# Optimization experiments

Measured on AMD Instinct MI355X. Metric: run time of the kernel, lower is better.

Reference implementation:

```python
import jax, jax.numpy as jnp
import numpy as np
from jax import lax

B, NS, SL, NF = 1024, 9, 36, 7
H, DM, DH, FFN = 2, 128, 64, 2048
EPS = 1e-5


def setup_inputs():
    ks = jax.random.split(jax.random.key(0), 12)
    r = lambda i, shape, s=0.05: jax.random.normal(ks[i], shape, dtype=jnp.float32) * s
    return {
        "x": jax.random.normal(ks[0], (B, NS, SL, NF), dtype=jnp.float32),
        "W_g1": r(1, (NS, 64)), "b_g1": jnp.zeros((64,), jnp.float32),
        "W_g2": r(2, (64, DM)), "b_g2": jnp.zeros((DM,), jnp.float32),
        "conv1_w": r(3, (64, NF, 5)), "conv1_b": jnp.zeros((64,), jnp.float32),
        "conv2_w": r(4, (DM, 64, 3)), "conv2_b": jnp.zeros((DM,), jnp.float32),
        "bn_g": jnp.ones((DM,), jnp.float32), "bn_b": jnp.zeros((DM,), jnp.float32),
        "bn_m": jnp.zeros((DM,), jnp.float32), "bn_v": jnp.ones((DM,), jnp.float32),
        "in_proj_w": r(5, (2, 3 * DM, DM)), "in_proj_b": jnp.zeros((2, 3 * DM), jnp.float32),
        "out_proj_w": r(6, (2, DM, DM)), "out_proj_b": jnp.zeros((2, DM), jnp.float32),
        "ln1_g": jnp.ones((2, DM), jnp.float32), "ln1_b": jnp.zeros((2, DM), jnp.float32),
        "ln2_g": jnp.ones((2, DM), jnp.float32), "ln2_b": jnp.zeros((2, DM), jnp.float32),
        "ffn_w1": r(7, (2, FFN, DM)), "ffn_b1": jnp.zeros((2, FFN), jnp.float32),
        "ffn_w2": r(8, (2, DM, FFN)), "ffn_b2": jnp.zeros((2, DM), jnp.float32),
        "attn_w": r(9, (DM, 1)), "attn_b": jnp.zeros((1,), jnp.float32),
        "fc_w": r(10, (DM, 1)), "fc_b": jnp.zeros((1,), jnp.float32),
    }


def _ln(z, g, b):
    m = jnp.mean(z, -1, keepdims=True)
    v = jnp.mean(jnp.square(z - m), -1, keepdims=True)
    return (z - m) * lax.rsqrt(v + EPS) * g + b


def _gcn_agg(h):
    # Fully-connected 9-node graph (softmax(adj) > 0 everywhere, incl. self loops):
    # GCN norm deg=9 -> rows 0..8 become the mean of rows 0..8.
    # Remaining rows only receive the add_remaining_self_loops self loop (deg=1) -> identity.
    return h.at[:NS].set(jnp.mean(h[:NS], axis=0, keepdims=True))


def _forward(x, W_g1, b_g1, W_g2, b_g2, conv1_w, conv1_b, conv2_w, conv2_b,
             bn_g, bn_b, bn_m, bn_v, in_proj_w, in_proj_b, out_proj_w, out_proj_b,
             ln1_g, ln1_b, ln2_g, ln2_b, ffn_w1, ffn_b1, ffn_w2, ffn_b2,
             attn_w, attn_b, fc_w, fc_b):
    Bx = x.shape[0]
    # ---- GCN branch (edge weights from softmax(adj) are never used by GCNConv) ----
    xg = jnp.mean(x, axis=-1).reshape(Bx * SL, NS)                 # (B*36, 9)
    h = jax.nn.relu(_gcn_agg(xg @ W_g1) + b_g1)                    # (B*36, 64)
    h = jax.nn.relu(_gcn_agg(h @ W_g2) + b_g2)                     # (B*36, 128)
    x_gcn = h.reshape(Bx, SL, DM)
    # ---- conv branch ----
    xc = x.reshape(Bx * NS, NF, SL)
    dn = ("NCH", "OIH", "NCH")
    c = lax.conv_general_dilated(xc, conv1_w, (1,), [(2, 2)], dimension_numbers=dn) + conv1_b[:, None]
    c = lax.conv_general_dilated(c, conv2_w, (1,), [(1, 1)], dimension_numbers=dn) + conv2_b[:, None]
    c = (c - bn_m[:, None]) * lax.rsqrt(bn_v[:, None] + EPS) * bn_g[:, None] + bn_b[:, None]
    # AdaptiveAvgPool1d(36) on length-36 input is identity; eval-mode dropout is identity.
    s = c.reshape(Bx, NS, DM, SL).mean(axis=1).transpose(0, 2, 1)  # (B, 36, 128) batch-first
    # ---- post-LN transformer encoder (torch defaults, eval mode) ----
    scale = 1.0 / np.sqrt(DH).astype(np.float32)
    for i in range(2):
        qkv = s @ in_proj_w[i].T + in_proj_b[i]                    # (B, 36, 384)
        q, k, v = jnp.split(qkv, 3, axis=-1)
        q = q.reshape(Bx, SL, H, DH).transpose(0, 2, 1, 3)
        k = k.reshape(Bx, SL, H, DH).transpose(0, 2, 1, 3)
        v = v.reshape(Bx, SL, H, DH).transpose(0, 2, 1, 3)
        a = jax.nn.softmax(jnp.einsum("bhqd,bhkd->bhqk", q, k) * scale, axis=-1)
        o = jnp.einsum("bhqk,bhkd->bhqd", a, v).transpose(0, 2, 1, 3).reshape(Bx, SL, DM)
        o = o @ out_proj_w[i].T + out_proj_b[i]
        s = _ln(s + o, ln1_g[i], ln1_b[i])
        f = jax.nn.relu(s @ ffn_w1[i].T + ffn_b1[i]) @ ffn_w2[i].T + ffn_b2[i]
        s = _ln(s + f, ln2_g[i], ln2_b[i])
    # ---- fuse branches + attention pooling + head ----
    s = s + x_gcn
    aw = jax.nn.softmax(s @ attn_w + attn_b, axis=1)               # softmax over seq dim
    pooled = jnp.sum(s * aw, axis=1)                               # (B, 128)
    out = pooled @ fc_w + fc_b                                     # (B, 1)
    return jnp.where(out >= 0, out, 0.1 * out)                     # LeakyReLU(0.1)


def reference(x, W_g1, b_g1, W_g2, b_g2, conv1_w, conv1_b, conv2_w, conv2_b,
              bn_g, bn_b, bn_m, bn_v, in_proj_w, in_proj_b, out_proj_w, out_proj_b,
              ln1_g, ln1_b, ln2_g, ln2_b, ffn_w1, ffn_b1, ffn_w2, ffn_b2,
              attn_w, attn_b, fc_w, fc_b):
    return _forward(x, W_g1, b_g1, W_g2, b_g2, conv1_w, conv1_b, conv2_w, conv2_b,
                    bn_g, bn_b, bn_m, bn_v, in_proj_w, in_proj_b, out_proj_w, out_proj_b,
                    ln1_g, ln1_b, ln2_g, ln2_b, ffn_w1, ffn_b1, ffn_w2, ffn_b2,
                    attn_w, attn_b, fc_w, fc_b)
```

## Files before the change

### kernel.cpp

```cpp
#include <hip/hip_runtime.h>
#include <math.h>

#define EPSV   1e-5f

typedef __attribute__((ext_vector_type(8))) short bf16x8;
typedef __attribute__((ext_vector_type(4))) float f32x4;

__device__ __forceinline__ short f2bf(float f){
    unsigned u = __float_as_uint(f);
    u += 0x7fffu + ((u >> 16) & 1u);
    return (short)(u >> 16);
}
__device__ __forceinline__ f32x4 mfma16(bf16x8 a, bf16x8 b, f32x4 c){
    return __builtin_amdgcn_mfma_f32_16x16x32_bf16(a, b, c, 0, 0, 0);
}
__device__ __forceinline__ bf16x8 ldfrag(const short* base, int row, int kbyte, int rowBytes){
    int byte = row * rowBytes + kbyte;
    byte ^= (row & 7) << 4;
    return *(const bf16x8*)((const char*)base + byte);
}
__device__ __forceinline__ bf16x8 ldfragG(const short* base, int row, int kbyte, int rowBytes){
    return *(const bf16x8*)((const char*)base + (size_t)row * rowBytes + kbyte);
}
__device__ __forceinline__ void stswz(short* base, int row, int col, int rowBytes, short v){
    int byte = row * rowBytes + col * 2;
    byte ^= (row & 7) << 4;
    *(short*)((char*)base + byte) = v;
}

__global__ __launch_bounds__(256) void cvt_all(
    const float* __restrict__ ipw, const float* __restrict__ opw,
    const float* __restrict__ fw1, const float* __restrict__ fw2,
    short* __restrict__ dst)
{
    int i = (blockIdx.x * 256 + threadIdx.x) * 4;
    if (i >= 1179648) return;
    const float* src; int off;
    if (i < 98304)       { src = ipw; off = i; }
    else if (i < 131072) { src = opw; off = i - 98304; }
    else if (i < 655360) { src = fw1; off = i - 131072; }
    else {
        int o  = i - 655360;
        int L  = o >> 18;
        int oo = o & 262143;
        int s0 = oo & 7;
        int lg = (oo >> 3) & 3;
        int c  = (oo >> 5) & 127;
        int grp = oo >> 12;
        int n  = grp * 32 + ((s0 >> 2) << 4) + lg * 4;
        src = fw2; off = L * 262144 + c * 2048 + n;
        float4 v = *(const float4*)(src + off);
        short4 s;
        s.x = f2bf(v.x); s.y = f2bf(v.y); s.z = f2bf(v.z); s.w = f2bf(v.w);
        *(short4*)(dst + i) = s;
        return;
    }
    float4 v = *(const float4*)(src + off);
    short4 s;
    s.x = f2bf(v.x); s.y = f2bf(v.y); s.z = f2bf(v.z); s.w = f2bf(v.w);
    *(short4*)(dst + i) = s;
}

__global__ __launch_bounds__(256) void gcn_all(
    const float* __restrict__ x,
    const float* __restrict__ Wg1, const float* __restrict__ bg1,
    const float* __restrict__ Wg2, const float* __restrict__ bg2,
    float* __restrict__ xgcn)
{
    int tid = threadIdx.x;
    if (blockIdx.x == 18432) {
        __shared__ float xgm[9];
        __shared__ float h1s[64];
        if (tid < 9) {
            float s = 0.f;
            for (int r = 0; r < 9; ++r) {
                const float* xp = x + (r * 9 + tid) * 7;
                #pragma unroll
                for (int f = 0; f < 7; ++f) s += xp[f];
            }
            xgm[tid] = s * (1.f / 63.f);
        }
        __syncthreads();
        if (tid < 64) {
            float acc = bg1[tid];
            #pragma unroll
            for (int j = 0; j < 9; ++j) acc += xgm[j] * Wg1[j * 64 + tid];
            h1s[tid] = fmaxf(acc, 0.f);
        }
        __syncthreads();
        if (tid < 128) {
            float acc = bg2[tid];
            #pragma unroll 8
            for (int c = 0; c < 64; ++c) acc += h1s[c] * Wg2[c * 128 + tid];
            float v = fmaxf(acc, 0.f);
            for (int r = 0; r < 9; ++r) xgcn[r * 128 + tid] = v;
        }
        return;
    }

    __shared__ float xg[2][9];
    __shared__ float h1[2][64];
    int ri = tid >> 7;
    int tr = tid & 127;
    int row = blockIdx.x * 2 + ri;

    if (tr < 9) {
        const float* xp = x + (row * 9 + tr) * 7;
        float s = 0.f;
        #pragma unroll
        for (int f = 0; f < 7; ++f) s += xp[f];
        xg[ri][tr] = s * (1.f / 7.f);
    }
    __syncthreads();
    if (tr < 64) {
        float acc = bg1[tr];
        #pragma unroll
        for (int j = 0; j < 9; ++j) acc += xg[ri][j] * Wg1[j * 64 + tr];
        h1[ri][tr] = fmaxf(acc, 0.f);
    }
    __syncthreads();
    if (row >= 9) {
        float acc = bg2[tr];
        #pragma unroll 8
        for (int c = 0; c < 64; ++c) acc += h1[ri][c] * Wg2[c * 128 + tr];
        xgcn[row * 128 + tr] = fmaxf(acc, 0.f);
    }
}

__global__ __launch_bounds__(256) void conv_branch(
    const float* __restrict__ x,
    const float* __restrict__ w1, const float* __restrict__ cb1,
    const float* __restrict__ w2, const float* __restrict__ cb2,
    const float* __restrict__ bng, const float* __restrict__ bnb,
    const float* __restrict__ bnm, const float* __restrict__ bnv,
    float* __restrict__ sbuf)
{
    __shared__ float xm[7 * 40];
    __shared__ float w1s[64 * 35];
    __shared__ float o1[64 * 38];
    int tid = threadIdx.x;
    int b = blockIdx.x;

    for (int idx = tid; idx < 7 * 40; idx += 256) xm[idx] = 0.f;
    for (int idx = tid; idx < 64 * 38; idx += 256) o1[idx] = 0.f;
    for (int idx = tid; idx < 2240; idx += 256) w1s[idx] = w1[idx];
    __syncthreads();

    const float* xb = x + (size_t)b * 2268;
    for (int idx = tid; idx < 252; idx += 256) {
        int f = idx / 36, l = idx - f * 36;
        float s = 0.f;
        #pragma unroll
        for (int n = 0; n < 9; ++n) s += xb[n * 252 + idx];
        xm[f * 40 + l + 2] = s * (1.f / 9.f);
    }
    __syncthreads();

    {
        int o = tid & 63, lh = tid >> 6;
        int l0 = lh * 9;
        float acc[9];
        float bias = cb1[o];
        #pragma unroll
        for (int r = 0; r < 9; ++r) acc[r] = bias;
        #pragma unroll
        for (int i = 0; i < 7; ++i) {
            #pragma unroll
            for (int k = 0; k < 5; ++k) {
                float w = w1s[o * 35 + i * 5 + k];
                const float* xrow = &xm[i * 40 + l0 + k];
                #pragma unroll
                for (int r = 0; r < 9; ++r) acc[r] += w * xrow[r];
            }
        }
        #pragma unroll
        for (int r = 0; r < 9; ++r) o1[o * 38 + l0 + r + 1] = acc[r];
    }
    __syncthreads();

    {
        int c = tid & 127, lh = tid >> 7;
        int l0 = lh * 18;
        float acc[18];
        #pragma unroll
        for (int r = 0; r < 18; ++r) acc[r] = 0.f;
        const float* w2c = w2 + c * 192;
        for (int i = 0; i < 64; ++i) {
            float wa = w2c[i * 3 + 0], wb = w2c[i * 3 + 1], wc = w2c[i * 3 + 2];
            const float* orow = &o1[i * 38 + l0];
            #pragma unroll
            for (int r = 0; r < 18; ++r)
                acc[r] += wa * orow[r] + wb * orow[r + 1] + wc * orow[r + 2];
        }
        float scale = bng[c] * rsqrtf(bnv[c] + EPSV);
        float shift = bnb[c] - bnm[c] * scale;
        float bias  = cb2[c];
        float* sb = sbuf + ((size_t)b * 36 + l0) * 128 + c;
        #pragma unroll
        for (int r = 0; r < 18; ++r)
            sb[r * 128] = (acc[r] + bias) * scale + shift;
    }
}

__global__ __launch_bounds__(256, 2) void attn_mfma(
    float* __restrict__ sbuf,
    const short* __restrict__ ipwb, const float* __restrict__ ipb,
    const short* __restrict__ opwb, const float* __restrict__ opb,
    const float* __restrict__ l1g, const float* __restrict__ l1b)
{
    __shared__ short Sb[48 * 128] __attribute__((aligned(16)));
    __shared__ char  U[38912]     __attribute__((aligned(16)));
    __shared__ float scf[36 * 40];
    short* Qb = (short*)U;
    short* Kb = (short*)(U + 6144);
    short* Vt = (short*)(U + 12288);
    short* Pb = (short*)(U + 20480);
    short* Hb = (short*)(U + 26624);

    const int tid  = threadIdx.x;
    const int wid  = tid >> 6;
    const int lane = tid & 63;
    const int lr   = lane & 15;
    const int lg   = lane >> 4;
    const int kbse = lg * 16;

    float* sg = sbuf + (size_t)blockIdx.x * 4608;
    const f32x4 fzero = {0.f, 0.f, 0.f, 0.f};

    for (int idx = tid; idx < 4608; idx += 256) {
        int r = idx >> 7, c = idx & 127;
        stswz(Sb, r, c, 256, f2bf(sg[idx]));
    }
    for (int idx = tid; idx < 1536; idx += 256)
        stswz(Sb, 36 + (idx >> 7), idx & 127, 256, 0);
    for (int idx = tid; idx < 1024; idx += 256)
        stswz(Vt, idx >> 4, 48 + (idx & 15), 128, 0);
    for (int idx = tid; idx < 768; idx += 256)
        stswz(Pb, 36 + (idx >> 6), idx & 63, 128, 0);
    __syncthreads();

    for (int h = 0; h < 2; ++h) {
        {
            f32x4 acc[3][3];
            #pragma unroll
            for (int a = 0; a < 3; ++a)
                #pragma unroll
                for (int m = 0; m < 3; ++m) acc[a][m] = fzero;
            const int wrow0 = h * 64 + wid * 16 + lr;
            #pragma unroll
            for (int ks = 0; ks < 4; ++ks) {
                bf16x8 a0 = ldfrag(Sb,      lr, ks * 64 + kbse, 256);
                bf16x8 a1 = ldfrag(Sb, 16 + lr, ks * 64 + kbse, 256);
                bf16x8 a2 = ldfrag(Sb, 32 + lr, ks * 64 + kbse, 256);
                #pragma unroll
                for (int mat = 0; mat < 3; ++mat) {
                    bf16x8 bf = ldfragG(ipwb, mat * 128 + wrow0, ks * 64 + kbse, 256);
                    acc[mat][0] = mfma16(a0, bf, acc[mat][0]);
                    acc[mat][1] = mfma16(a1, bf, acc[mat][1]);
                    acc[mat][2] = mfma16(a2, bf, acc[mat][2]);
                }
            }
            int col = wid * 16 + lr;
            #pragma unroll
            for (int mat = 0; mat < 3; ++mat) {
                float bias = ipb[mat * 128 + h * 64 + col];
                #pragma unroll
                for (int mt = 0; mt < 3; ++mt) {
                    f32x4 c4 = acc[mat][mt];
                    if (mat == 0) {
                        #pragma unroll
                        for (int j = 0; j < 4; ++j)
                            stswz(Qb, mt * 16 + lg * 4 + j, col, 128, f2bf(c4[j] + bias));
                    } else if (mat == 1) {
                        #pragma unroll
                        for (int j = 0; j < 4; ++j)
                            stswz(Kb, mt * 16 + lg * 4 + j, col, 128, f2bf(c4[j] + bias));
                    } else {
                        int rbase = mt * 16 + lg * 4;
                        short4 s4;
                        s4.x = f2bf(rbase + 0 < 36 ? c4[0] + bias : 0.f);
                        s4.y = f2bf(rbase + 1 < 36 ? c4[1] + bias : 0.f);
                        s4.z = f2bf(rbase + 2 < 36 ? c4[2] + bias : 0.f);
                        s4.w = f2bf(rbase + 3 < 36 ? c4[3] + bias : 0.f);
                        int byte = col * 128 + rbase * 2;
                        byte ^= (col & 7) << 4;
                        *(short4*)((char*)Vt + byte) = s4;
                    }
                }
            }
        }
        __syncthreads();

        for (int t = wid; t < 9; t += 4) {
            int mt = t / 3, nt = t - mt * 3;
            f32x4 acc = fzero;
            #pragma unroll
            for (int ks = 0; ks < 2; ++ks) {
                bf16x8 a = ldfrag(Qb, mt * 16 + lr, ks * 64 + kbse, 128);
                bf16x8 b = ldfrag(Kb, nt * 16 + lr, ks * 64 + kbse, 128);
                acc = mfma16(a, b, acc);
            }
            int col = nt * 16 + lr;
            if (col < 36) {
                #pragma unroll
                for (int j = 0; j < 4; ++j) {
                    int r = mt * 16 + lg * 4 + j;
                    if (r < 36) scf[r * 40 + col] = acc[j] * 0.125f;
                }
            }
        }
        __syncthreads();

        {
            int g = tid >> 2, e = tid & 3;
            if (g < 36) {
                float v[9];
                float mx = -1e30f;
                #pragma unroll
                for (int i = 0; i < 9; ++i) { v[i] = scf[g * 40 + e * 9 + i]; mx = fmaxf(mx, v[i]); }
                mx = fmaxf(mx, __shfl_xor(mx, 1));
                mx = fmaxf(mx, __shfl_xor(mx, 2));
                float ssum = 0.f;
                #pragma unroll
                for (int i = 0; i < 9; ++i) { v[i] = __expf(v[i] - mx); ssum += v[i]; }
                ssum += __shfl_xor(ssum, 1);
                ssum += __shfl_xor(ssum, 2);
                float inv = 1.f / ssum;
                #pragma unroll
                for (int i = 0; i < 9; ++i)
                    stswz(Pb, g, e * 9 + i, 128, f2bf(v[i] * inv));
                #pragma unroll
                for (int i = 0; i < 7; ++i)
                    stswz(Pb, g, 36 + e * 7 + i, 128, 0);
            }
        }
        __syncthreads();

        {
            f32x4 oacc[3] = {fzero, fzero, fzero};
            #pragma unroll
            for (int ks = 0; ks < 2; ++ks) {
                bf16x8 b = ldfrag(Vt, wid * 16 + lr, ks * 64 + kbse, 128);
                #pragma unroll
                for (int mt = 0; mt < 3; ++mt) {
                    bf16x8 a = ldfrag(Pb, mt * 16 + lr, ks * 64 + kbse, 128);
                    oacc[mt] = mfma16(a, b, oacc[mt]);
                }
            }
            int col = h * 64 + wid * 16 + lr;
            #pragma unroll
            for (int mt = 0; mt < 3; ++mt)
                #pragma unroll
                for (int j = 0; j < 4; ++j)
                    stswz(Hb, mt * 16 + lg * 4 + j, col, 256, f2bf(oacc[mt][j]));
        }
        __syncthreads();
    }

    float z[3][2][4];
    {
        f32x4 pacc[3][2];
        #pragma unroll
        for (int m = 0; m < 3; ++m) { pacc[m][0] = fzero; pacc[m][1] = fzero; }
        #pragma unroll
        for (int ks = 0; ks < 4; ++ks) {
            bf16x8 a0 = ldfrag(Hb,      lr, ks * 64 + kbse, 256);
            bf16x8 a1 = ldfrag(Hb, 16 + lr, ks * 64 + kbse, 256);
            bf16x8 a2 = ldfrag(Hb, 32 + lr, ks * 64 + kbse, 256);
            #pragma unroll
            for (int t = 0; t < 2; ++t) {
                bf16x8 b = ldfragG(opwb, (wid * 2 + t) * 16 + lr, ks * 64 + kbse, 256);
                pacc[0][t] = mfma16(a0, b, pacc[0][t]);
                pacc[1][t] = mfma16(a1, b, pacc[1][t]);
                pacc[2][t] = mfma16(a2, b, pacc[2][t]);
            }
        }
        #pragma unroll
        for (int t = 0; t < 2; ++t) {
            int col = (wid * 2 + t) * 16 + lr;
            float bias = opb[col];
            #pragma unroll
            for (int mt = 0; mt < 3; ++mt)
                #pragma unroll
                for (int j = 0; j < 4; ++j) {
                    int r = mt * 16 + lg * 4 + j;
                    z[mt][t][j] = (r < 36) ? pacc[mt][t][j] + bias + sg[r * 128 + col] : 0.f;
                }
        }
    }
    {
        float* part = scf;
        #pragma unroll
        for (int mt = 0; mt < 3; ++mt)
            #pragma unroll
            for (int j = 0; j < 4; ++j) {
                int r = mt * 16 + lg * 4 + j;
                float s  = z[mt][0][j] + z[mt][1][j];
                float ss = z[mt][0][j] * z[mt][0][j] + z[mt][1][j] * z[mt][1][j];
                s  += __shfl_xor(s, 1);  s  += __shfl_xor(s, 2);
                s  += __shfl_xor(s, 4);  s  += __shfl_xor(s, 8);
                ss += __shfl_xor(ss, 1); ss += __shfl_xor(ss, 2);
                ss += __shfl_xor(ss, 4); ss += __shfl_xor(ss, 8);
                if (lr == 0 && r < 36) { part[r * 8 + wid] = s; part[r * 8 + 4 + wid] = ss; }
            }
    }
    __syncthreads();
    {
        const float* part = scf;
        #pragma unroll
        for (int mt = 0; mt < 3; ++mt)
            #pragma unroll
            for (int j = 0; j < 4; ++j) {
                int r = mt * 16 + lg * 4 + j;
                if (r < 36) {
                    float s  = part[r * 8 + 0] + part[r * 8 + 1] + part[r * 8 + 2] + part[r * 8 + 3];
                    float ss = part[r * 8 + 4] + part[r * 8 + 5] + part[r * 8 + 6] + part[r * 8 + 7];
                    float mean = s * (1.f / 128.f);
                    float rstd = rsqrtf(ss * (1.f / 128.f) - mean * mean + EPSV);
                    #pragma unroll
                    for (int t = 0; t < 2; ++t) {
                        int col = (wid * 2 + t) * 16 + lr;
                        float v = (z[mt][t][j] - mean) * rstd * l1g[col] + l1b[col];
                        sg[r * 128 + col] = v;
                    }
                }
            }
    }
}

__global__ __launch_bounds__(256, 2) void ffn_lds(
    float* __restrict__ sres,
    const short* __restrict__ fw1b, const float* __restrict__ fb1,
    const short* __restrict__ fw2p, const float* __restrict__ fb2,
    const float* __restrict__ l2g, const float* __restrict__ l2b)
{
    __shared__ short Wbuf[2][16384] __attribute__((aligned(16)));

    const int tid  = threadIdx.x;
    const int wid  = tid >> 6;
    const int lane = tid & 63;
    const int lr   = lane & 15;
    const int lg   = lane >> 4;
    const size_t row0 = (size_t)blockIdx.x * 64 + wid * 16;
    const f32x4 fzero = {0.f, 0.f, 0.f, 0.f};

    bf16x8 sfrag[4];
    {
        const float* sp = sres + (row0 + lr) * 128;
        #pragma unroll
        for (int ks = 0; ks < 4; ++ks) {
            float4 lo = *(const float4*)(sp + ks * 32 + lg * 8);
            float4 hi = *(const float4*)(sp + ks * 32 + lg * 8 + 4);
            bf16x8 f;
            f[0] = f2bf(lo.x); f[1] = f2bf(lo.y); f[2] = f2bf(lo.z); f[3] = f2bf(lo.w);
            f[4] = f2bf(hi.x); f[5] = f2bf(hi.y); f[6] = f2bf(hi.z); f[7] = f2bf(hi.w);
            sfrag[ks] = f;
        }
    }

    f32x4 facc[8];
    #pragma unroll
    for (int ct = 0; ct < 8; ++ct) facc[ct] = fzero;

    bf16x8 g1[4], g2[4];
    #pragma unroll
    for (int i2 = 0; i2 < 4; ++i2) {
        int fid = tid + 256 * i2;
        g1[i2] = *(const bf16x8*)((const char*)fw1b + fid * 16);
        g2[i2] = *(const bf16x8*)((const char*)fw2p + fid * 16);
    }
    #pragma unroll
    for (int i2 = 0; i2 < 4; ++i2) {
        int fid = tid + 256 * i2;
        int swz = (fid * 16) ^ ((((fid >> 4) & 7)) << 4);
        *(bf16x8*)((char*)&Wbuf[0][0] + swz)          = g1[i2];
        *(bf16x8*)((char*)&Wbuf[0][8192] + fid * 16)  = g2[i2];
    }

    #pragma unroll 2
    for (int q = 0; q < 32; ++q) {
        if (q < 31) {
            const char* b1p = (const char*)fw1b + (q + 1) * 16384;
            const char* b2p = (const char*)fw2p + (q + 1) * 16384;
            #pragma unroll
            for (int i2 = 0; i2 < 4; ++i2) {
                int fid = tid + 256 * i2;
                g1[i2] = *(const bf16x8*)(b1p + fid * 16);
                g2[i2] = *(const bf16x8*)(b2p + fid * 16);
            }
        }
        __syncthreads();
        const short* W1l = &Wbuf[q & 1][0];
        const short* W2l = &Wbuf[q & 1][8192];

        f32x4 hacc[4];
        #pragma unroll
        for (int nt = 0; nt < 4; ++nt) hacc[nt] = fzero;
        #pragma unroll
        for (int ks = 0; ks < 4; ++ks) {
            #pragma unroll
            for (int nt = 0; nt < 4; ++nt) {
                bf16x8 a = ldfrag(W1l, nt * 16 + lr, ks * 64 + lg * 16, 256);
                hacc[nt] = mfma16(a, sfrag[ks], hacc[nt]);
            }
        }

        const int nbase = q * 64;
        bf16x8 hf[2];
        #pragma unroll
        for (int ksn = 0; ksn < 2; ++ksn) {
            float4 bA = *(const float4*)(fb1 + nbase + ksn * 32 + lg * 4);
            float4 bB = *(const float4*)(fb1 + nbase + ksn * 32 + 16 + lg * 4);
            bf16x8 h;
            h[0] = f2bf(fmaxf(hacc[ksn * 2][0]     + bA.x, 0.f));
            h[1] = f2bf(fmaxf(hacc[ksn * 2][1]     + bA.y, 0.f));
            h[2] = f2bf(fmaxf(hacc[ksn * 2][2]     + bA.z, 0.f));
            h[3] = f2bf(fmaxf(hacc[ksn * 2][3]     + bA.w, 0.f));
            h[4] = f2bf(fmaxf(hacc[ksn * 2 + 1][0] + bB.x, 0.f));
            h[5] = f2bf(fmaxf(hacc[ksn * 2 + 1][1] + bB.y, 0.f));
            h[6] = f2bf(fmaxf(hacc[ksn * 2 + 1][2] + bB.z, 0.f));
            h[7] = f2bf(fmaxf(hacc[ksn * 2 + 1][3] + bB.w, 0.f));
            hf[ksn] = h;
        }

        #pragma unroll
        for (int ksn = 0; ksn < 2; ++ksn)
            #pragma unroll
            for (int ct = 0; ct < 8; ++ct) {
                bf16x8 b2 = *(const bf16x8*)(W2l +
                              ((ksn * 128 + ct * 16 + lr) * 4 + lg) * 8);
                facc[ct] = mfma16(hf[ksn], b2, facc[ct]);
            }

        if (q < 31) {
            char* d1 = (char*)&Wbuf[(q + 1) & 1][0];
            char* d2 = (char*)&Wbuf[(q + 1) & 1][8192];
            #pragma unroll
            for (int i2 = 0; i2 < 4; ++i2) {
                int fid = tid + 256 * i2;
                int swz = (fid * 16) ^ ((((fid >> 4) & 7)) << 4);
                *(bf16x8*)(d1 + swz)        = g1[i2];
                *(bf16x8*)(d2 + fid * 16)   = g2[i2];
            }
        }
    }

    float zv[8][4];
    #pragma unroll
    for (int ct = 0; ct < 8; ++ct) {
        int c = ct * 16 + lr;
        float b2v = fb2[c];
        #pragma unroll
        for (int j = 0; j < 4; ++j)
            zv[ct][j] = facc[ct][j] + b2v + sres[(row0 + lg * 4 + j) * 128 + c];
    }
    #pragma unroll
    for (int j = 0; j < 4; ++j) {
        float s = 0.f, sq = 0.f;
        #pragma unroll
        for (int ct = 0; ct < 8; ++ct) { s += zv[ct][j]; sq += zv[ct][j] * zv[ct][j]; }
        s  += __shfl_xor(s, 1);  s  += __shfl_xor(s, 2);
        s  += __shfl_xor(s, 4);  s  += __shfl_xor(s, 8);
        sq += __shfl_xor(sq, 1); sq += __shfl_xor(sq, 2);
        sq += __shfl_xor(sq, 4); sq += __shfl_xor(sq, 8);
        float mean = s * (1.f / 128.f);
        float rstd = rsqrtf(sq * (1.f / 128.f) - mean * mean + EPSV);
        float* og = sres + (row0 + lg * 4 + j) * 128;
        #pragma unroll
        for (int ct = 0; ct < 8; ++ct) {
            int c = ct * 16 + lr;
            og[c] = (zv[ct][j] - mean) * rstd * l2g[c] + l2b[c];
        }
    }
}

__global__ __launch_bounds__(128) void pool_head(
    const float* __restrict__ sbuf, const float* __restrict__ xgcn,
    const float* __restrict__ aww, const float* __restrict__ awb,
    const float* __restrict__ fcw, const float* __restrict__ fcb,
    float* __restrict__ out)
{
    __shared__ float sl[36][128];
    __shared__ float zz[36];
    __shared__ float p[128];
    int tid = threadIdx.x;
    int b = blockIdx.x;
    const float* sg = sbuf + (size_t)b * 4608;
    const float* gg = xgcn + (size_t)b * 4608;
    for (int idx = tid; idx < 4608; idx += 128)
        sl[0][idx] = sg[idx] + gg[idx];
    __syncthreads();
    if (tid < 36) {
        float acc = awb[0];
        #pragma unroll
        for (int j = 0; j < 128; j += 4) {
            float4 s4 = *(const float4*)&sl[tid][j];
            float4 w4 = *(const float4*)(aww + j);
            acc += s4.x * w4.x + s4.y * w4.y + s4.z * w4.z + s4.w * w4.w;
        }
        zz[tid] = acc;
    }
    __syncthreads();
    if (tid == 0) {
        float m = -1e30f;
        for (int k = 0; k < 36; ++k) m = fmaxf(m, zz[k]);
        float ssum = 0.f;
        for (int k = 0; k < 36; ++k) ssum += __expf(zz[k] - m);
        float inv = 1.f / ssum;
        for (int k = 0; k < 36; ++k) zz[k] = __expf(zz[k] - m) * inv;
    }
    __syncthreads();
    {
        float acc = 0.f;
        for (int l = 0; l < 36; ++l) acc += sl[l][tid] * zz[l];
        p[tid] = acc;
    }
    __syncthreads();
    if (tid == 0) {
        float acc = fcb[0];
        for (int dd = 0; dd < 128; ++dd) acc += p[dd] * fcw[dd];
        out[b] = acc >= 0.f ? acc : 0.1f * acc;
    }
}

extern "C" void kernel_launch(void* const* d_in, const int* in_sizes, int n_in,
                              void* d_out, int out_size, void* d_ws, size_t ws_size,
                              hipStream_t stream)
{
    const float* x   = (const float*)d_in[0];
    const float* Wg1 = (const float*)d_in[1];
    const float* bg1 = (const float*)d_in[2];
    const float* Wg2 = (const float*)d_in[3];
    const float* bg2 = (const float*)d_in[4];
    const float* c1w = (const float*)d_in[5];
    const float* c1b = (const float*)d_in[6];
    const float* c2w = (const float*)d_in[7];
    const float* c2b = (const float*)d_in[8];
    const float* bng = (const float*)d_in[9];
    const float* bnb = (const float*)d_in[10];
    const float* bnm = (const float*)d_in[11];
    const float* bnv = (const float*)d_in[12];
    const float* ipw = (const float*)d_in[13];
    const float* ipb = (const float*)d_in[14];
    const float* opw = (const float*)d_in[15];
    const float* opb = (const float*)d_in[16];
    const float* l1g = (const float*)d_in[17];
    const float* l1b = (const float*)d_in[18];
    const float* l2g = (const float*)d_in[19];
    const float* l2b = (const float*)d_in[20];
    const float* fw1 = (const float*)d_in[21];
    const float* fb1 = (const float*)d_in[22];
    const float* fw2 = (const float*)d_in[23];
    const float* fb2 = (const float*)d_in[24];
    const float* aww = (const float*)d_in[25];
    const float* awb = (const float*)d_in[26];
    const float* fcw = (const float*)d_in[27];
    const float* fcb = (const float*)d_in[28];
    float* out = (float*)d_out;

    float* sbuf = (float*)d_ws;
    float* xgcn = sbuf + (size_t)1024 * 36 * 128;
    short* wb   = (short*)(xgcn + (size_t)1024 * 36 * 128);
    short* ipwb = wb;
    short* opwb = wb + 98304;
    short* fw1b = wb + 131072;
    short* fw2p = wb + 655360;

    cvt_all<<<1152, 256, 0, stream>>>(ipw, opw, fw1, fw2, wb);
    gcn_all<<<18433, 256, 0, stream>>>(x, Wg1, bg1, Wg2, bg2, xgcn);
    conv_branch<<<1024, 256, 0, stream>>>(x, c1w, c1b, c2w, c2b,
                                          bng, bnb, bnm, bnv, sbuf);
    for (int i = 0; i < 2; ++i) {
        attn_mfma<<<1024, 256, 0, stream>>>(sbuf,
            ipwb + (size_t)i * 49152, ipb + (size_t)i * 384,
            opwb + (size_t)i * 16384, opb + (size_t)i * 128,
            l1g + (size_t)i * 128, l1b + (size_t)i * 128);
        ffn_lds<<<576, 256, 0, stream>>>(sbuf,
            fw1b + (size_t)i * 262144, fb1 + (size_t)i * 2048,
            fw2p + (size_t)i * 262144, fb2 + (size_t)i * 128,
            l2g + (size_t)i * 128, l2b + (size_t)i * 128);
    }
    pool_head<<<1024, 128, 0, stream>>>(sbuf, xgcn, aww, awb, fcw, fcb, out);
}
```

Before: 358.2 us.

## Use two-wave FFN blocks with 32 rows per wave to reuse weight fragments

The FFN kernel now runs 128 threads (2 waves) per block, and each wave handles two 16-row tiles, so every LDS weight fragment feeds two MFMAs. This halves LDS weight reads per MFMA and manually unrolls the double-buffer loop with constant buffer indices. Each thread now loads twice as many global chunks, and register pressure rises with the doubled accumulators. Occupancy may fall because the launch bounds drop to 128 threads with min 1 block. The attention kernel also stops zeroing the padding rows of Sb and Pb, which risks stale LDS data in padded rows if they are ever read.

After: 417.4 us. 1.17x slower.

```diff
diff --git a/kernel.cpp b/kernel.cpp
--- a/kernel.cpp
+++ b/kernel.cpp
@@ -231,12 +231,8 @@
         int r = idx >> 7, c = idx & 127;
         stswz(Sb, r, c, 256, f2bf(sg[idx]));
     }
-    for (int idx = tid; idx < 1536; idx += 256)
-        stswz(Sb, 36 + (idx >> 7), idx & 127, 256, 0);
     for (int idx = tid; idx < 1024; idx += 256)
         stswz(Vt, idx >> 4, 48 + (idx & 15), 128, 0);
-    for (int idx = tid; idx < 768; idx += 256)
-        stswz(Pb, 36 + (idx >> 6), idx & 63, 128, 0);
     __syncthreads();
 
     for (int h = 0; h < 2; ++h) {
@@ -428,7 +424,7 @@
     }
 }
 
-__global__ __launch_bounds__(256, 2) void ffn_lds(
+__global__ __launch_bounds__(128, 1) void ffn_v4(
     float* __restrict__ sres,
     const short* __restrict__ fw1b, const float* __restrict__ fb1,
     const short* __restrict__ fw2p, const float* __restrict__ fb2,
@@ -441,12 +437,13 @@
     const int lane = tid & 63;
     const int lr   = lane & 15;
     const int lg   = lane >> 4;
-    const size_t row0 = (size_t)blockIdx.x * 64 + wid * 16;
+    const size_t row0 = (size_t)blockIdx.x * 64 + wid * 32;
     const f32x4 fzero = {0.f, 0.f, 0.f, 0.f};
 
-    bf16x8 sfrag[4];
-    {
-        const float* sp = sres + (row0 + lr) * 128;
+    bf16x8 sfrag[2][4];
+    #pragma unroll
+    for (int rt = 0; rt < 2; ++rt) {
+        const float* sp = sres + (row0 + rt * 16 + lr) * 128;
         #pragma unroll
         for (int ks = 0; ks < 4; ++ks) {
             float4 lo = *(const float4*)(sp + ks * 32 + lg * 8);
@@ -454,122 +451,140 @@
             bf16x8 f;
             f[0] = f2bf(lo.x); f[1] = f2bf(lo.y); f[2] = f2bf(lo.z); f[3] = f2bf(lo.w);
             f[4] = f2bf(hi.x); f[5] = f2bf(hi.y); f[6] = f2bf(hi.z); f[7] = f2bf(hi.w);
-            sfrag[ks] = f;
-        }
-    }
-
-    f32x4 facc[8];
+            sfrag[rt][ks] = f;
+        }
+    }
+
+    f32x4 facc[2][8];
     #pragma unroll
-    for (int ct = 0; ct < 8; ++ct) facc[ct] = fzero;
-
-    bf16x8 g1[4], g2[4];
+    for (int rt = 0; rt < 2; ++rt)
+        #pragma unroll
+        for (int ct = 0; ct < 8; ++ct) facc[rt][ct] = fzero;
+
+    bf16x8 g1[8], g2[8];
     #pragma unroll
-    for (int i2 = 0; i2 < 4; ++i2) {
-        int fid = tid + 256 * i2;
-        g1[i2] = *(const bf16x8*)((const char*)fw1b + fid * 16);
-        g2[i2] = *(const bf16x8*)((const char*)fw2p + fid * 16);
+    for (int i = 0; i < 8; ++i) {
+        int fid = tid + 128 * i;
+        g1[i] = *(const bf16x8*)((const char*)fw1b + fid * 16);
+        g2[i] = *(const bf16x8*)((const char*)fw2p + fid * 16);
     }
     #pragma unroll
-    for (int i2 = 0; i2 < 4; ++i2) {
-        int fid = tid + 256 * i2;
-        int swz = (fid * 16) ^ ((((fid >> 4) & 7)) << 4);
-        *(bf16x8*)((char*)&Wbuf[0][0] + swz)          = g1[i2];
-        *(bf16x8*)((char*)&Wbuf[0][8192] + fid * 16)  = g2[i2];
-    }
-
-    #pragma unroll 2
-    for (int q = 0; q < 32; ++q) {
-        if (q < 31) {
-            const char* b1p = (const char*)fw1b + (q + 1) * 16384;
-            const char* b2p = (const char*)fw2p + (q + 1) * 16384;
-            #pragma unroll
-            for (int i2 = 0; i2 < 4; ++i2) {
-                int fid = tid + 256 * i2;
-                g1[i2] = *(const bf16x8*)(b1p + fid * 16);
-                g2[i2] = *(const bf16x8*)(b2p + fid * 16);
-            }
-        }
-        __syncthreads();
-        const short* W1l = &Wbuf[q & 1][0];
-        const short* W2l = &Wbuf[q & 1][8192];
-
-        f32x4 hacc[4];
-        #pragma unroll
-        for (int nt = 0; nt < 4; ++nt) hacc[nt] = fzero;
-        #pragma unroll
-        for (int ks = 0; ks < 4; ++ks) {
-            #pragma unroll
-            for (int nt = 0; nt < 4; ++nt) {
-                bf16x8 a = ldfrag(W1l, nt * 16 + lr, ks * 64 + lg * 16, 256);
-                hacc[nt] = mfma16(a, sfrag[ks], hacc[nt]);
-            }
-        }
-
-        const int nbase = q * 64;
-        bf16x8 hf[2];
-        #pragma unroll
-        for (int ksn = 0; ksn < 2; ++ksn) {
-            float4 bA = *(const float4*)(fb1 + nbase + ksn * 32 + lg * 4);
-            float4 bB = *(const float4*)(fb1 + nbase + ksn * 32 + 16 + lg * 4);
-            bf16x8 h;
-            h[0] = f2bf(fmaxf(hacc[ksn * 2][0]     + bA.x, 0.f));
-            h[1] = f2bf(fmaxf(hacc[ksn * 2][1]     + bA.y, 0.f));
-            h[2] = f2bf(fmaxf(hacc[ksn * 2][2]     + bA.z, 0.f));
-            h[3] = f2bf(fmaxf(hacc[ksn * 2][3]     + bA.w, 0.f));
-            h[4] = f2bf(fmaxf(hacc[ksn * 2 + 1][0] + bB.x, 0.f));
-            h[5] = f2bf(fmaxf(hacc[ksn * 2 + 1][1] + bB.y, 0.f));
-            h[6] = f2bf(fmaxf(hacc[ksn * 2 + 1][2] + bB.z, 0.f));
-            h[7] = f2bf(fmaxf(hacc[ksn * 2 + 1][3] + bB.w, 0.f));
-            hf[ksn] = h;
-        }
-
-        #pragma unroll
-        for (int ksn = 0; ksn < 2; ++ksn)
-            #pragma unroll
-            for (int ct = 0; ct < 8; ++ct) {
-                bf16x8 b2 = *(const bf16x8*)(W2l +
-                              ((ksn * 128 + ct * 16 + lr) * 4 + lg) * 8);
-                facc[ct] = mfma16(hf[ksn], b2, facc[ct]);
-            }
-
-        if (q < 31) {
-            char* d1 = (char*)&Wbuf[(q + 1) & 1][0];
-            char* d2 = (char*)&Wbuf[(q + 1) & 1][8192];
-            #pragma unroll
-            for (int i2 = 0; i2 < 4; ++i2) {
-                int fid = tid + 256 * i2;
-                int swz = (fid * 16) ^ ((((fid >> 4) & 7)) << 4);
-                *(bf16x8*)(d1 + swz)        = g1[i2];
-                *(bf16x8*)(d2 + fid * 16)   = g2[i2];
-            }
-        }
-    }
-
-    float zv[8][4];
+    for (int i = 0; i < 8; ++i) {
+        int fid = tid + 128 * i;
+        int swz = (fid * 16) ^ (((fid >> 4) & 7) << 4);
+        *(bf16x8*)((char*)&Wbuf[0][0] + swz)         = g1[i];
+        *(bf16x8*)((char*)&Wbuf[0][8192] + fid * 16) = g2[i];
+    }
+
+#define FFN_CHUNK(Q, CUR, NXT)                                                    \
+    {                                                                             \
+        const int q = (Q);                                                        \
+        if (q < 31) {                                                             \
+            const char* b1p = (const char*)fw1b + (q + 1) * 16384;                \
+            const char* b2p = (const char*)fw2p + (q + 1) * 16384;                \
+            _Pragma("unroll")                                                     \
+            for (int i = 0; i < 8; ++i) {                                         \
+                int fid = tid + 128 * i;                                          \
+                g1[i] = *(const bf16x8*)(b1p + fid * 16);                         \
+                g2[i] = *(const bf16x8*)(b2p + fid * 16);                         \
+            }                                                                     \
+        }                                                                         \
+        __syncthreads();                 \
+        const short* W1l = &Wbuf[CUR][0];                                         \
+        const short* W2l = &Wbuf[CUR][8192];                                      \
+              \
+        f32x4 hacc[2][4];                                                         \
+        _Pragma("unroll")                                                         \
+        for (int rt = 0; rt < 2; ++rt)                                            \
+            _Pragma("unroll")                                                     \
+            for (int nt = 0; nt < 4; ++nt) hacc[rt][nt] = fzero;                  \
+        _Pragma("unroll")                                                         \
+        for (int ks = 0; ks < 4; ++ks)                                            \
+            _Pragma("unroll")                                                     \
+            for (int nt = 0; nt < 4; ++nt) {                                      \
+                bf16x8 a = ldfrag(W1l, nt * 16 + lr, ks * 64 + lg * 16, 256);     \
+                hacc[0][nt] = mfma16(a, sfrag[0][ks], hacc[0][nt]);               \
+                hacc[1][nt] = mfma16(a, sfrag[1][ks], hacc[1][nt]);               \
+            }                                                                     \
+        \
+        bf16x8 hf[2][2];                                                          \
+        _Pragma("unroll")                                                         \
+        for (int ksn = 0; ksn < 2; ++ksn) {                                       \
+            float4 bA = *(const float4*)(fb1 + q * 64 + ksn * 32 + lg * 4);       \
+            float4 bB = *(const float4*)(fb1 + q * 64 + ksn * 32 + 16 + lg * 4);  \
+            _Pragma("unroll")                                                     \
+            for (int rt = 0; rt < 2; ++rt) {                                      \
+                bf16x8 h;                                                         \
+                h[0] = f2bf(fmaxf(hacc[rt][ksn * 2][0]     + bA.x, 0.f));         \
+                h[1] = f2bf(fmaxf(hacc[rt][ksn * 2][1]     + bA.y, 0.f));         \
+                h[2] = f2bf(fmaxf(hacc[rt][ksn * 2][2]     + bA.z, 0.f));         \
+                h[3] = f2bf(fmaxf(hacc[rt][ksn * 2][3]     + bA.w, 0.f));         \
+                h[4] = f2bf(fmaxf(hacc[rt][ksn * 2 + 1][0] + bB.x, 0.f));         \
+                h[5] = f2bf(fmaxf(hacc[rt][ksn * 2 + 1][1] + bB.y, 0.f));         \
+                h[6] = f2bf(fmaxf(hacc[rt][ksn * 2 + 1][2] + bB.z, 0.f));         \
+                h[7] = f2bf(fmaxf(hacc[rt][ksn * 2 + 1][3] + bB.w, 0.f));         \
+                hf[rt][ksn] = h;                                                  \
+            }                                                                     \
+        }                                                                         \
+                     \
+        _Pragma("unroll")                                                         \
+        for (int ksn = 0; ksn < 2; ++ksn)                                         \
+            _Pragma("unroll")                                                     \
+            for (int ct = 0; ct < 8; ++ct) {                                      \
+                bf16x8 b2 = *(const bf16x8*)(W2l +                                \
+                              ((ksn * 128 + ct * 16 + lr) * 4 + lg) * 8);         \
+                facc[0][ct] = mfma16(hf[0][ksn], b2, facc[0][ct]);                \
+                facc[1][ct] = mfma16(hf[1][ksn], b2, facc[1][ct]);                \
+            }                                                                     \
+        if (q < 31) {                                                             \
+            char* d1 = (char*)&Wbuf[NXT][0];                                      \
+            char* d2 = (char*)&Wbuf[NXT][8192];                                   \
+            _Pragma("unroll")                                                     \
+            for (int i = 0; i < 8; ++i) {                                         \
+                int fid = tid + 128 * i;                                          \
+                int swz = (fid * 16) ^ (((fid >> 4) & 7) << 4);                   \
+                *(bf16x8*)(d1 + swz)        = g1[i];                              \
+                *(bf16x8*)(d2 + fid * 16)   = g2[i];                              \
+            }                                                                     \
+        }                                                                         \
+    }
+
+    #pragma unroll 1
+    for (int qq = 0; qq < 16; ++qq) {
+        FFN_CHUNK(2 * qq,     0, 1)
+        FFN_CHUNK(2 * qq + 1, 1, 0)
+    }
+#undef FFN_CHUNK
+
     #pragma unroll
-    for (int ct = 0; ct < 8; ++ct) {
-        int c = ct * 16 + lr;
-        float b2v = fb2[c];
-        #pragma unroll
-        for (int j = 0; j < 4; ++j)
-            zv[ct][j] = facc[ct][j] + b2v + sres[(row0 + lg * 4 + j) * 128 + c];
-    }
-    #pragma unroll
-    for (int j = 0; j < 4; ++j) {
-        float s = 0.f, sq = 0.f;
-        #pragma unroll
-        for (int ct = 0; ct < 8; ++ct) { s += zv[ct][j]; sq += zv[ct][j] * zv[ct][j]; }
-        s  += __shfl_xor(s, 1);  s  += __shfl_xor(s, 2);
-        s  += __shfl_xor(s, 4);  s  += __shfl_xor(s, 8);
-        sq += __shfl_xor(sq, 1); sq += __shfl_xor(sq, 2);
-        sq += __shfl_xor(sq, 4); sq += __shfl_xor(sq, 8);
-        float mean = s * (1.f / 128.f);
-        float rstd = rsqrtf(sq * (1.f / 128.f) - mean * mean + EPSV);
-        float* og = sres + (row0 + lg * 4 + j) * 128;
+    for (int rt = 0; rt < 2; ++rt) {
+        const size_t rowb = row0 + rt * 16;
+        float zv[8][4];
         #pragma unroll
         for (int ct = 0; ct < 8; ++ct) {
             int c = ct * 16 + lr;
-            og[c] = (zv[ct][j] - mean) * rstd * l2g[c] + l2b[c];
+            float b2v = fb2[c];
+            #pragma unroll
+            for (int j = 0; j < 4; ++j)
+                zv[ct][j] = facc[rt][ct][j] + b2v + sres[(rowb + lg * 4 + j) * 128 + c];
+        }
+        #pragma unroll
+        for (int j = 0; j < 4; ++j) {
+            float s = 0.f, sq = 0.f;
+            #pragma unroll
+            for (int ct = 0; ct < 8; ++ct) { s += zv[ct][j]; sq += zv[ct][j] * zv[ct][j]; }
+            s  += __shfl_xor(s, 1);  s  += __shfl_xor(s, 2);
+            s  += __shfl_xor(s, 4);  s  += __shfl_xor(s, 8);
+            sq += __shfl_xor(sq, 1); sq += __shfl_xor(sq, 2);
+            sq += __shfl_xor(sq, 4); sq += __shfl_xor(sq, 8);
+            float mean = s * (1.f / 128.f);
+            float rstd = rsqrtf(sq * (1.f / 128.f) - mean * mean + EPSV);
+            float* og = sres + (rowb + lg * 4 + j) * 128;
+            #pragma unroll
+            for (int ct = 0; ct < 8; ++ct) {
+                int c = ct * 16 + lr;
+                og[c] = (zv[ct][j] - mean) * rstd * l2g[c] + l2b[c];
+            }
         }
     }
 }
@@ -675,7 +690,7 @@
             ipwb + (size_t)i * 49152, ipb + (size_t)i * 384,
             opwb + (size_t)i * 16384, opb + (size_t)i * 128,
             l1g + (size_t)i * 128, l1b + (size_t)i * 128);
-        ffn_lds<<<576, 256, 0, stream>>>(sbuf,
+        ffn_v4<<<576, 128, 0, stream>>>(sbuf,
             fw1b + (size_t)i * 262144, fb1 + (size_t)i * 2048,
             fw2p + (size_t)i * 262144, fb2 + (size_t)i * 128,
             l2g + (size_t)i * 128, l2b + (size_t)i * 128);
```
